# Kernel tuning notes

Measured on AMD Instinct MI355X. Metric: run time of the kernel, lower is better.

The kernel has to match this reference:

```python
import jax, jax.numpy as jnp
import numpy as np

B, D, S = 4096, 1024, 1024

def setup_inputs() -> dict:
    key = jax.random.key(0)
    ks = jax.random.split(key, 12)
    u = lambda k, shp: jax.random.uniform(k, shp, jnp.float32, -0.05, 0.05)
    return {
        "inputs": jax.random.normal(ks[0], (B, D), jnp.float32),
        "h0": jax.random.normal(ks[1], (B, S), jnp.float32),
        "c0": jax.random.normal(ks[2], (B, S), jnp.float32),
        "w_f": u(ks[3], (D, S)), "u_f": u(ks[4], (S, S)), "b_f": u(ks[5], (S,)),
        "w_i": u(ks[6], (D, S)), "u_i": u(ks[7], (S, S)), "b_i": u(ks[8], (S,)),
        "w_o": u(ks[9], (D, S)), "u_o": u(ks[10], (S, S)), "b_o": u(ks[11], (S,)),
    }

def reference(inputs, h0, c0, w_f, u_f, b_f, w_i, u_i, b_i, w_o, u_o, b_o):
    # Faithful to the original: input_cell reuses the FORGET gate weights and
    # sigmoid (not tanh, not w_c) -- a quirk of the source module.
    pre_f = inputs @ w_f + h0 @ u_f + b_f          # [B, S]
    forget_gate = jax.nn.sigmoid(pre_f)
    input_gate = jax.nn.sigmoid(inputs @ w_i + h0 @ u_i + b_i)
    output_gate = jax.nn.sigmoid(inputs @ w_o + h0 @ u_o + b_o)
    input_cell = jax.nn.sigmoid(pre_f)             # same pre-activation as forget gate
    c_new = forget_gate * c0 + input_cell * input_gate
    h_new = output_gate * jnp.tanh(c_new)
    return (h_new, c_new)
```

## Files before the change

kernel.cpp:

```cpp
#include <hip/hip_runtime.h>
#include <cstdint>
#include <cstddef>


typedef __attribute__((ext_vector_type(8))) short bf16x8;
typedef __attribute__((ext_vector_type(4))) float f32x4;
typedef __attribute__((ext_vector_type(8))) short s16x8;
typedef __attribute__((ext_vector_type(4))) float f32x4v;

#define MROWS 4096
#define KD    1024
#define KALL  2048
#define NC    1024

__device__ __forceinline__ short f2bf(float f) {
    uint32_t u = __builtin_bit_cast(uint32_t, f);
    u += 0x7fffu + ((u >> 16) & 1u);
    return (short)(u >> 16);
}

__global__ void cvt_bf16_kernel(const float* __restrict__ x,
                                const float* __restrict__ h,
                                short* __restrict__ ab) {
    int b = blockIdx.x;
    const float* in;
    int coff;
    if (b < 2048) { in = x; coff = 0; }
    else          { in = h; coff = KD; b -= 2048; }
    const int i = (b * 256 + threadIdx.x) * 8;
    const int row = i >> 10, col = i & 1023;
    f32x4v a = *(const f32x4v*)(in + i);
    f32x4v c = *(const f32x4v*)(in + i + 4);
    s16x8 o;
    o[0] = f2bf(a[0]); o[1] = f2bf(a[1]); o[2] = f2bf(a[2]); o[3] = f2bf(a[3]);
    o[4] = f2bf(c[0]); o[5] = f2bf(c[1]); o[6] = f2bf(c[2]); o[7] = f2bf(c[3]);
    *(s16x8*)(ab + (size_t)row * KALL + coff + col) = o;
}

struct W6 { const float* src[6]; };

__global__ void pack_w_kernel(W6 p, short* __restrict__ bp) {
    __shared__ short tile[32][33];
    const int z = blockIdx.z;
    const float* __restrict__ w = p.src[z];
    const int g    = (z < 3) ? z : z - 3;
    const int koff = (z < 3) ? 0 : KD;
    const int tx = threadIdx.x & 31;
    const int ty = threadIdx.x >> 5;
    const int kbase = blockIdx.y * 32;
    const int nbase = blockIdx.x * 32;
#pragma unroll
    for (int r = 0; r < 4; ++r) {
        int k = kbase + ty + r * 8;
        tile[ty + r * 8][tx] = f2bf(w[k * NC + nbase + tx]);
    }
    __syncthreads();
#pragma unroll
    for (int r = 0; r < 4; ++r) {
        const int n = nbase + ty + r * 8;
        const int pcol = ((n >> 4) * 3 + g) * 16 + (n & 15);
        bp[(size_t)pcol * KALL + koff + kbase + tx] = tile[tx][ty + r * 8];
    }
}

__global__ __launch_bounds__(512, 2)
void lstm_gemm_kernel(const short* __restrict__ Ab, const short* __restrict__ Bp,
                      const float* __restrict__ bf_, const float* __restrict__ bi_,
                      const float* __restrict__ bo_,
                      const float* __restrict__ c0,
                      float* __restrict__ outH, float* __restrict__ outC) {
    __shared__ __align__(16) char lds[2][57344];

    const int tid  = threadIdx.x;
    const int lane = tid & 63;
    const int wave = tid >> 6;
    const int wr   = wave >> 2;
    const int wc   = wave & 3;
    const int m0   = blockIdx.y * 256;
    const int np0  = blockIdx.x * 192;

    const int l15 = lane & 15;
    const int q   = lane >> 4;

    f32x4 acc[8][3] = {};

    const int srow = tid >> 2;
    const int skel = ((tid & 3) ^ ((tid >> 3) & 3)) * 8;
    const short* aPtr[4];
#pragma unroll
    for (int l = 0; l < 4; ++l) {
        const int ks = l >> 1, mh = l & 1;
        aPtr[l] = Ab + (size_t)(m0 + mh * 128 + srow) * KALL + ks * 32 + skel;
    }
    const short* bPtr[3];
#pragma unroll
    for (int w = 0; w < 3; ++w) {
        const int pbyte = w * 8192 + tid * 16;
        const int ks  = pbyte / 12288;
        const int rem = pbyte - ks * 12288;
        const int row = rem >> 6;
        const int slot = (rem >> 4) & 3;
        bPtr[w] = Bp + (size_t)(np0 + row) * KALL + ks * 32 +
                  ((slot ^ ((row >> 1) & 3)) * 8);
    }

    int aOffV[8];
#pragma unroll
    for (int m = 0; m < 8; ++m) {
        const int r = m * 16 + l15;
        aOffV[m] = wr * 8192 + r * 64 + ((q ^ ((r >> 1) & 3)) << 4);
    }
    int bOffV[3];
#pragma unroll
    for (int g = 0; g < 3; ++g) {
        const int r = wc * 48 + g * 16 + l15;
        bOffV[g] = 32768 + r * 64 + ((q ^ ((r >> 1) & 3)) << 4);
    }

#define GLDS(SRC, DOFF)                                                      \
    __builtin_amdgcn_global_load_lds(                                        \
        (const __attribute__((address_space(1))) unsigned int*)(uintptr_t)(SRC), \
        (__attribute__((address_space(3))) unsigned int*)(uintptr_t)         \
            (Ls + (DOFF) + tid * 16), 16, 0, 0)

#define BAR    __builtin_amdgcn_s_barrier()
#define SCHED0 __builtin_amdgcn_sched_barrier(0)
#define LGKM0  asm volatile("s_waitcnt lgkmcnt(0)" ::: "memory")

#define MFMA12(MB)                                                           \
    {                                                                        \
        __builtin_amdgcn_s_setprio(1);                                       \
        _Pragma("unroll")                                                    \
        for (int mm = 0; mm < 4; ++mm)                                       \
            _Pragma("unroll")                                                \
            for (int g = 0; g < 3; ++g)                                      \
                acc[(MB) + mm][g] = __builtin_amdgcn_mfma_f32_16x16x32_bf16( \
                    af[mm], bg[g], acc[(MB) + mm][g], 0, 0, 0);              \
        __builtin_amdgcn_s_setprio(0);                                       \
    }

    {
        char* Ls = lds[0];
        GLDS(aPtr[0], 0);      GLDS(aPtr[1], 8192);
        GLDS(bPtr[0], 32768);  GLDS(bPtr[1], 40960);
        GLDS(aPtr[2], 16384);  GLDS(aPtr[3], 24576);
        GLDS(bPtr[2], 49152);
    }
    asm volatile("s_waitcnt vmcnt(3)" ::: "memory");
    BAR;

    bf16x8 af[4], bg[3];

    for (int t = 0; t < 31; ++t) {
        const char* L = lds[t & 1];
        char* Ls = lds[(t + 1) & 1];
        const int kb = (t + 1) * 64;

#pragma unroll
        for (int mm = 0; mm < 4; ++mm) af[mm] = *(const bf16x8*)(L + aOffV[mm]);
#pragma unroll
        for (int g = 0; g < 3; ++g)    bg[g] = *(const bf16x8*)(L + bOffV[g]);
        GLDS(aPtr[0] + kb, 0);
        GLDS(aPtr[1] + kb, 8192);
        SCHED0;
        BAR;
        LGKM0;
        SCHED0;
        MFMA12(0);
        BAR;

#pragma unroll
        for (int mm = 0; mm < 4; ++mm)
            af[mm] = *(const bf16x8*)(L + aOffV[4 + mm]);
        GLDS(bPtr[0] + kb, 32768);
        GLDS(bPtr[1] + kb, 40960);
        SCHED0;
        BAR;
        LGKM0;
        SCHED0;
        MFMA12(4);
        asm volatile("s_waitcnt vmcnt(4)" ::: "memory");
        BAR;

#pragma unroll
        for (int mm = 0; mm < 4; ++mm)
            af[mm] = *(const bf16x8*)(L + 16384 + aOffV[mm]);
#pragma unroll
        for (int g = 0; g < 3; ++g)
            bg[g] = *(const bf16x8*)(L + 12288 + bOffV[g]);
        GLDS(aPtr[2] + kb, 16384);
        GLDS(aPtr[3] + kb, 24576);
        SCHED0;
        BAR;
        LGKM0;
        SCHED0;
        MFMA12(0);
        BAR;

#pragma unroll
        for (int mm = 0; mm < 4; ++mm)
            af[mm] = *(const bf16x8*)(L + 16384 + aOffV[4 + mm]);
        GLDS(bPtr[2] + kb, 49152);
        SCHED0;
        BAR;
        LGKM0;
        SCHED0;
        MFMA12(4);
        asm volatile("s_waitcnt vmcnt(3)" ::: "memory");
        BAR;
    }

    {
        const char* L = lds[1];
#pragma unroll
        for (int mm = 0; mm < 4; ++mm) af[mm] = *(const bf16x8*)(L + aOffV[mm]);
#pragma unroll
        for (int g = 0; g < 3; ++g)    bg[g] = *(const bf16x8*)(L + bOffV[g]);
        SCHED0; BAR; LGKM0; SCHED0;
        MFMA12(0);
        BAR;
#pragma unroll
        for (int mm = 0; mm < 4; ++mm)
            af[mm] = *(const bf16x8*)(L + aOffV[4 + mm]);
        SCHED0; BAR; LGKM0; SCHED0;
        MFMA12(4);
        asm volatile("s_waitcnt vmcnt(0)" ::: "memory");
        BAR;
#pragma unroll
        for (int mm = 0; mm < 4; ++mm)
            af[mm] = *(const bf16x8*)(L + 16384 + aOffV[mm]);
#pragma unroll
        for (int g = 0; g < 3; ++g)
            bg[g] = *(const bf16x8*)(L + 12288 + bOffV[g]);
        SCHED0; BAR; LGKM0; SCHED0;
        MFMA12(0);
        BAR;
#pragma unroll
        for (int mm = 0; mm < 4; ++mm)
            af[mm] = *(const bf16x8*)(L + 16384 + aOffV[4 + mm]);
        LGKM0; SCHED0;
        MFMA12(4);
    }

    const int rj  = q * 4;
    const int col = blockIdx.x * 64 + wc * 16 + l15;
    const float bfv = bf_[col], biv = bi_[col], bov = bo_[col];
#pragma unroll
    for (int m = 0; m < 8; ++m) {
        const f32x4 pf = acc[m][0];
        const f32x4 pi = acc[m][1];
        const f32x4 po = acc[m][2];
#pragma unroll
        for (int j = 0; j < 4; ++j) {
            const int row = m0 + wr * 128 + m * 16 + rj + j;
            const float fg = 1.f / (1.f + __expf(-(pf[j] + bfv)));
            const float ig = 1.f / (1.f + __expf(-(pi[j] + biv)));
            const float og = 1.f / (1.f + __expf(-(po[j] + bov)));
            const float cv = c0[row * NC + col];
            const float cn = fg * cv + fg * ig;
            const float e  = __expf(-2.f * cn);
            const float th = (1.f - e) / (1.f + e);
            outH[row * NC + col] = og * th;
            outC[row * NC + col] = cn;
        }
    }
#undef GLDS
#undef BAR
#undef SCHED0
#undef LGKM0
#undef MFMA12
}

extern "C" void kernel_launch(void* const* d_in, const int* in_sizes, int n_in,
                              void* d_out, int out_size, void* d_ws, size_t ws_size,
                              hipStream_t stream) {
    const float* inputs = (const float*)d_in[0];
    const float* h0     = (const float*)d_in[1];
    const float* c0     = (const float*)d_in[2];
    const float* w_f    = (const float*)d_in[3];
    const float* u_f    = (const float*)d_in[4];
    const float* b_f    = (const float*)d_in[5];
    const float* w_i    = (const float*)d_in[6];
    const float* u_i    = (const float*)d_in[7];
    const float* b_i    = (const float*)d_in[8];
    const float* w_o    = (const float*)d_in[9];
    const float* u_o    = (const float*)d_in[10];
    const float* b_o    = (const float*)d_in[11];

    float* outH = (float*)d_out;
    float* outC = outH + (size_t)MROWS * NC;

    char* ws = (char*)d_ws;
    short* Ab = (short*)(ws);
    short* Bp = (short*)(ws + (16u << 20));

    cvt_bf16_kernel<<<4096, 256, 0, stream>>>(inputs, h0, Ab);

    W6 p;
    p.src[0] = w_f; p.src[1] = w_i; p.src[2] = w_o;
    p.src[3] = u_f; p.src[4] = u_i; p.src[5] = u_o;
    pack_w_kernel<<<dim3(32, 32, 6), 256, 0, stream>>>(p, Bp);

    dim3 grid(16, 16);
    lstm_gemm_kernel<<<grid, 512, 0, stream>>>(
        Ab, Bp, b_f, b_i, b_o, c0, outH, outC);
}
```

Baseline: 76.22 us.

## Merge MFMA phases to halve barriers per K-step in fused LSTM GEMM

Restructures the main loop so that each half-K slab loads all 8 A fragments and 3 B fragments at once and issues 24 MFMAs, instead of splitting the work into two 12-MFMA phases with a barrier between them. Barriers per iteration drop from eight to two, and the vmcnt waits move to the start of each phase. This cuts synchronisation stalls and gives the scheduler longer MFMA runs. In exchange it uses more VGPRs for the wider A fragment array and prefetch interleaving becomes coarser, and the correctness of the shared-memory reuse now depends on the reordered barrier placement.

```diff
diff --git a/kernel.cpp b/kernel.cpp
--- a/kernel.cpp
+++ b/kernel.cpp
@@ -126,16 +126,17 @@
 #define BAR    __builtin_amdgcn_s_barrier()
 #define SCHED0 __builtin_amdgcn_sched_barrier(0)
 #define LGKM0  asm volatile("s_waitcnt lgkmcnt(0)" ::: "memory")
-
-#define MFMA12(MB)                                                           \
+#define WAITV(N) asm volatile("s_waitcnt vmcnt(" #N ")" ::: "memory")
+
+#define MFMA24(AF, BG)                                                       \
     {                                                                        \
         __builtin_amdgcn_s_setprio(1);                                       \
         _Pragma("unroll")                                                    \
-        for (int mm = 0; mm < 4; ++mm)                                       \
+        for (int mm = 0; mm < 8; ++mm)                                       \
             _Pragma("unroll")                                                \
             for (int g = 0; g < 3; ++g)                                      \
-                acc[(MB) + mm][g] = __builtin_amdgcn_mfma_f32_16x16x32_bf16( \
-                    af[mm], bg[g], acc[(MB) + mm][g], 0, 0, 0);              \
+                acc[mm][g] = __builtin_amdgcn_mfma_f32_16x16x32_bf16(        \
+                    AF[mm], BG[g], acc[mm][g], 0, 0, 0);                     \
         __builtin_amdgcn_s_setprio(0);                                       \
     }
 
@@ -146,100 +147,73 @@
         GLDS(aPtr[2], 16384);  GLDS(aPtr[3], 24576);
         GLDS(bPtr[2], 49152);
     }
-    asm volatile("s_waitcnt vmcnt(3)" ::: "memory");
-    BAR;
-
-    bf16x8 af[4], bg[3];
+
+    bf16x8 af[8], bg[3];
 
     for (int t = 0; t < 31; ++t) {
         const char* L = lds[t & 1];
         char* Ls = lds[(t + 1) & 1];
         const int kb = (t + 1) * 64;
 
-#pragma unroll
-        for (int mm = 0; mm < 4; ++mm) af[mm] = *(const bf16x8*)(L + aOffV[mm]);
+        WAITV(3);
+        BAR;
+        SCHED0;
+#pragma unroll
+        for (int mm = 0; mm < 8; ++mm) af[mm] = *(const bf16x8*)(L + aOffV[mm]);
 #pragma unroll
         for (int g = 0; g < 3; ++g)    bg[g] = *(const bf16x8*)(L + bOffV[g]);
         GLDS(aPtr[0] + kb, 0);
         GLDS(aPtr[1] + kb, 8192);
-        SCHED0;
-        BAR;
-        LGKM0;
-        SCHED0;
-        MFMA12(0);
-        BAR;
-
-#pragma unroll
-        for (int mm = 0; mm < 4; ++mm)
-            af[mm] = *(const bf16x8*)(L + aOffV[4 + mm]);
         GLDS(bPtr[0] + kb, 32768);
         GLDS(bPtr[1] + kb, 40960);
         SCHED0;
-        BAR;
-        LGKM0;
-        SCHED0;
-        MFMA12(4);
-        asm volatile("s_waitcnt vmcnt(4)" ::: "memory");
-        BAR;
-
-#pragma unroll
-        for (int mm = 0; mm < 4; ++mm)
+        LGKM0;
+        SCHED0;
+        MFMA24(af, bg);
+
+        WAITV(4);
+        BAR;
+        SCHED0;
+#pragma unroll
+        for (int mm = 0; mm < 8; ++mm)
             af[mm] = *(const bf16x8*)(L + 16384 + aOffV[mm]);
 #pragma unroll
         for (int g = 0; g < 3; ++g)
             bg[g] = *(const bf16x8*)(L + 12288 + bOffV[g]);
         GLDS(aPtr[2] + kb, 16384);
         GLDS(aPtr[3] + kb, 24576);
-        SCHED0;
-        BAR;
-        LGKM0;
-        SCHED0;
-        MFMA12(0);
-        BAR;
-
-#pragma unroll
-        for (int mm = 0; mm < 4; ++mm)
-            af[mm] = *(const bf16x8*)(L + 16384 + aOffV[4 + mm]);
         GLDS(bPtr[2] + kb, 49152);
         SCHED0;
-        BAR;
-        LGKM0;
-        SCHED0;
-        MFMA12(4);
-        asm volatile("s_waitcnt vmcnt(3)" ::: "memory");
-        BAR;
+        LGKM0;
+        SCHED0;
+        MFMA24(af, bg);
     }
 
     {
         const char* L = lds[1];
-#pragma unroll
-        for (int mm = 0; mm < 4; ++mm) af[mm] = *(const bf16x8*)(L + aOffV[mm]);
+        WAITV(3);
+        BAR;
+        SCHED0;
+#pragma unroll
+        for (int mm = 0; mm < 8; ++mm) af[mm] = *(const bf16x8*)(L + aOffV[mm]);
 #pragma unroll
         for (int g = 0; g < 3; ++g)    bg[g] = *(const bf16x8*)(L + bOffV[g]);
-        SCHED0; BAR; LGKM0; SCHED0;
-        MFMA12(0);
-        BAR;
-#pragma unroll
-        for (int mm = 0; mm < 4; ++mm)
-            af[mm] = *(const bf16x8*)(L + aOffV[4 + mm]);
-        SCHED0; BAR; LGKM0; SCHED0;
-        MFMA12(4);
-        asm volatile("s_waitcnt vmcnt(0)" ::: "memory");
-        BAR;
-#pragma unroll
-        for (int mm = 0; mm < 4; ++mm)
+        LGKM0;
+        SCHED0;
+        MFMA24(af, bg);
+
+        WAITV(0);
+        BAR;
+        SCHED0;
+#pragma unroll
+        for (int mm = 0; mm < 8; ++mm)
             af[mm] = *(const bf16x8*)(L + 16384 + aOffV[mm]);
 #pragma unroll
         for (int g = 0; g < 3; ++g)
             bg[g] = *(const bf16x8*)(L + 12288 + bOffV[g]);
-        SCHED0; BAR; LGKM0; SCHED0;
-        MFMA12(0);
-        BAR;
-#pragma unroll
-        for (int mm = 0; mm < 4; ++mm)
-            af[mm] = *(const bf16x8*)(L + 16384 + aOffV[4 + mm]);
-        LGKM0; SCHED0;
-        MFMA12(4);
+        LGKM0;
+        SCHED0;
+        MFMA24(af, bg);
     }
 
     const int rj  = q * 4;
@@ -268,7 +242,8 @@
 #undef BAR
 #undef SCHED0
 #undef LGKM0
-#undef MFMA12
+#undef WAITV
+#undef MFMA24
 }
 
 extern "C" void kernel_launch(void* const* d_in, const int* in_sizes, int n_in,
```

New measurement: 73.01 us. 1.04x faster.
